# Kernel optimization log

Hardware: AMD Instinct MI355X
Metric: run time of the kernel (lower is better)

## Reference

```python
import jax
import jax.numpy as jnp
import numpy as np

B, S, D, H, HID, E, TOPK = 1, 2048, 1024, 16, 4096, 8, 2
HEAD_DIM = D // H


def _layer_norm(x, g, b, eps=1e-5):
    mu = jnp.mean(x, axis=-1, keepdims=True)
    var = jnp.var(x, axis=-1, keepdims=True)
    return (x - mu) * jax.lax.rsqrt(var + eps) * g + b


def setup_inputs() -> dict:
    key = jax.random.key(0)
    ks = jax.random.split(key, 12)
    s = 0.02
    return {
        "x": jax.random.normal(ks[0], (B, S, D), jnp.float32),
        "ln1_g": jnp.ones((D,), jnp.float32),
        "ln1_b": jnp.zeros((D,), jnp.float32),
        "wq": jax.random.normal(ks[1], (D, D), jnp.float32) * s,
        "wk": jax.random.normal(ks[2], (D, D), jnp.float32) * s,
        "wv": jax.random.normal(ks[3], (D, D), jnp.float32) * s,
        "wo": jax.random.normal(ks[4], (D, D), jnp.float32) * s,
        "ln2_g": jnp.ones((D,), jnp.float32),
        "ln2_b": jnp.zeros((D,), jnp.float32),
        "w_gate": jax.random.normal(ks[5], (D, E), jnp.float32) * s,
        "w_eg": jax.random.normal(ks[6], (E, D, HID), jnp.float32) * s,
        "w_eu": jax.random.normal(ks[7], (E, D, HID), jnp.float32) * s,
        "w_ed": jax.random.normal(ks[8], (E, HID, D), jnp.float32) * s,
    }


def _attention(h, wq, wk, wv, wo):
    b, s, d = h.shape
    q = (h @ wq).reshape(b, s, H, HEAD_DIM).transpose(0, 2, 1, 3)
    k = (h @ wk).reshape(b, s, H, HEAD_DIM).transpose(0, 2, 1, 3)
    v = (h @ wv).reshape(b, s, H, HEAD_DIM).transpose(0, 2, 1, 3)
    scores = jnp.einsum("bhqd,bhkd->bhqk", q, k) / jnp.sqrt(jnp.asarray(HEAD_DIM, h.dtype))
    causal = jnp.tril(jnp.ones((s, s), bool))  # [s,s]
    scores = jnp.where(causal, scores, jnp.asarray(-1e30, h.dtype))
    attn = jax.nn.softmax(scores, axis=-1)
    out = jnp.einsum("bhqk,bhkd->bhqd", attn, v).transpose(0, 2, 1, 3).reshape(b, s, d)
    return out @ wo


def _moe(h, w_gate, w_eg, w_eu, w_ed):
    b, s, d = h.shape
    flat = h.reshape(-1, d)  # [T,D]
    logits = flat @ w_gate  # [T,E]
    scores = jax.nn.sigmoid(logits)
    top_val, top_idx = jax.lax.top_k(scores, TOPK)
    top_val = top_val / (jnp.sum(top_val, axis=-1, keepdims=True) + 1e-9)
    # per-token per-expert combine weight (0 for unrouted experts)
    combine = jnp.sum(jax.nn.one_hot(top_idx, E, dtype=flat.dtype) * top_val[..., None], axis=1)  # [T,E]
    g = jax.nn.silu(jnp.einsum("td,edh->eth", flat, w_eg))
    u = jnp.einsum("td,edh->eth", flat, w_eu)
    eo = jnp.einsum("eth,ehd->etd", g * u, w_ed)  # [E,T,D]
    out = jnp.einsum("etd,te->td", eo, combine)
    return out.reshape(b, s, d)


def reference(x, ln1_g, ln1_b, wq, wk, wv, wo, ln2_g, ln2_b, w_gate, w_eg, w_eu, w_ed):
    x = x + _attention(_layer_norm(x, ln1_g, ln1_b), wq, wk, wv, wo)
    x = x + _moe(_layer_norm(x, ln2_g, ln2_b), w_gate, w_eg, w_eu, w_ed)
    return x
```

## Files before the change

### kernel.cpp

```cpp
#include <hip/hip_runtime.h>
#include <hip/hip_bf16.h>
#include <stdint.h>

#define DI __device__ __forceinline__

typedef short bf16x8_t __attribute__((ext_vector_type(8)));
typedef float f32x4_t __attribute__((ext_vector_type(4)));

DI unsigned short f2bf(float f) {
  __hip_bfloat16 h = __float2bfloat16(f);
  unsigned short u;
  __builtin_memcpy(&u, &h, 2);
  return u;
}

DI uint32_t pk2(float a, float b) {
  return (uint32_t)f2bf(a) | ((uint32_t)f2bf(b) << 16);
}

DI f32x4_t mfma16(bf16x8_t a, bf16x8_t b, f32x4_t c) {
  return __builtin_amdgcn_mfma_f32_16x16x32_bf16(a, b, c, 0, 0, 0);
}

DI void gload16(const void* g, void* l) {
  __builtin_amdgcn_global_load_lds(
      (const __attribute__((address_space(1))) uint32_t*)g,
      (__attribute__((address_space(3))) uint32_t*)l, 16, 0, 0);
}

DI bf16x8_t frag(const unsigned short* base, int row, int hi) {
  return *(const bf16x8_t*)&base[row * 32 + ((hi ^ ((row >> 1) & 3)) * 8)];
}
DI int chunk_swz(int tid) { return ((tid & 3) ^ ((tid >> 3) & 3)) * 8; }

__global__ __launch_bounds__(256) void transpose_cvt(const float* __restrict__ in,
                                                     unsigned short* __restrict__ out,
                                                     int R, int C) {
  __shared__ float tile[64][65];
  const int tid = threadIdx.x;
  const int tx = tid & 15, ty = tid >> 4;
  const size_t zoff = (size_t)blockIdx.z * R * C;
  const int r0 = blockIdx.y * 64, c0 = blockIdx.x * 64;
#pragma unroll
  for (int i = 0; i < 4; ++i) {
    const int r = ty + i * 16;
    const float4 v = *(const float4*)(in + zoff + (size_t)(r0 + r) * C + c0 + tx * 4);
    tile[r][tx * 4 + 0] = v.x; tile[r][tx * 4 + 1] = v.y;
    tile[r][tx * 4 + 2] = v.z; tile[r][tx * 4 + 3] = v.w;
  }
  __syncthreads();
#pragma unroll
  for (int i = 0; i < 4; ++i) {
    const int r = ty + i * 16;
    ushort4 o;
    o.x = f2bf(tile[tx * 4 + 0][r]); o.y = f2bf(tile[tx * 4 + 1][r]);
    o.z = f2bf(tile[tx * 4 + 2][r]); o.w = f2bf(tile[tx * 4 + 3][r]);
    *(ushort4*)(out + zoff + (size_t)(c0 + r) * R + r0 + tx * 4) = o;
  }
}

__global__ __launch_bounds__(256) void ln_kernel(const float* __restrict__ x, const float* __restrict__ g,
                                                 const float* __restrict__ b, unsigned short* __restrict__ out) {
  const int row = blockIdx.x, tid = threadIdx.x;
  const int wid = tid >> 6, lane = tid & 63;
  const float4 v = *(const float4*)(x + (size_t)row * 1024 + tid * 4);
  float s = v.x + v.y + v.z + v.w;
  float s2 = v.x * v.x + v.y * v.y + v.z * v.z + v.w * v.w;
#pragma unroll
  for (int o = 1; o < 64; o <<= 1) { s += __shfl_xor(s, o); s2 += __shfl_xor(s2, o); }
  __shared__ float red[8];
  if (lane == 0) { red[wid] = s; red[4 + wid] = s2; }
  __syncthreads();
  const float ts = red[0] + red[1] + red[2] + red[3];
  const float ts2 = red[4] + red[5] + red[6] + red[7];
  const float mu = ts * 0.0009765625f;
  const float var = ts2 * 0.0009765625f - mu * mu;
  const float rs = rsqrtf(var + 1e-5f);
  const float4 gg = *(const float4*)(g + tid * 4);
  const float4 bb = *(const float4*)(b + tid * 4);
  ushort4 o4;
  o4.x = f2bf((v.x - mu) * rs * gg.x + bb.x);
  o4.y = f2bf((v.y - mu) * rs * gg.y + bb.y);
  o4.z = f2bf((v.z - mu) * rs * gg.z + bb.z);
  o4.w = f2bf((v.w - mu) * rs * gg.w + bb.w);
  *(ushort4*)(out + (size_t)row * 1024 + tid * 4) = o4;
}

template<int BN>
DI void gemm_loop(const unsigned short* aR0, const unsigned short* aR1,
                  const unsigned short* bR0, const unsigned short* bR1,
                  const int K, unsigned short* lds, const int tid,
                  f32x4_t (&acc)[4][BN / 32]) {
  constexpr int NF = BN / 32;
  unsigned short* ldsA = lds;
  unsigned short* ldsB = lds + 4096;
  const int wid = tid >> 6, lane = tid & 63, ln = lane & 15, hi = lane >> 4;
  const int wr = wid >> 1, wc = wid & 1;
  char* dstA0 = (char*)ldsA + wid * 1024;
  char* dstA1 = (char*)ldsA + 4096 + wid * 1024;
  char* dstB0 = (char*)ldsB + wid * 1024;
  char* dstB1 = (char*)ldsB + 4096 + wid * 1024;
  for (int k0 = 0; k0 < K; k0 += 32) {
    gload16(aR0 + k0, dstA0);
    gload16(aR1 + k0, dstA1);
    gload16(bR0 + k0, dstB0);
    if constexpr (BN == 128) gload16(bR1 + k0, dstB1);
    __syncthreads();
    bf16x8_t af[4];
#pragma unroll
    for (int mf = 0; mf < 4; ++mf)
      af[mf] = frag(ldsA, wr * 64 + mf * 16 + ln, hi);
#pragma unroll
    for (int nf = 0; nf < NF; ++nf) {
      bf16x8_t bfr = frag(ldsB, wc * (BN / 2) + nf * 16 + ln, hi);
#pragma unroll
      for (int mf = 0; mf < 4; ++mf)
        acc[mf][nf] = mfma16(af[mf], bfr, acc[mf][nf]);
    }
    __syncthreads();
  }
}

__global__ __launch_bounds__(256) void qkv_kernel(const unsigned short* __restrict__ h1,
                                                  const unsigned short* __restrict__ wqT,
                                                  const unsigned short* __restrict__ wkT,
                                                  const unsigned short* __restrict__ wvT,
                                                  unsigned short* __restrict__ qb,
                                                  unsigned short* __restrict__ kbf,
                                                  unsigned short* __restrict__ vt) {
  __shared__ unsigned short lds[128 * 32 + 128 * 32];
  const int tid = threadIdx.x;
  const int z = blockIdx.z;
  const unsigned short* BT = (z == 0) ? wqT : (z == 1) ? wkT : wvT;
  const int m0 = blockIdx.y * 128, n0 = blockIdx.x * 128;
  f32x4_t acc[4][4] = {};
  const int cs = chunk_swz(tid);
  const unsigned short* aR0 = h1 + (size_t)(m0 + (tid >> 2)) * 1024 + cs;
  const unsigned short* aR1 = aR0 + 64 * 1024;
  const unsigned short* bR0 = BT + (size_t)(n0 + (tid >> 2)) * 1024 + cs;
  const unsigned short* bR1 = bR0 + 64 * 1024;
  gemm_loop<128>(aR0, aR1, bR0, bR1, 1024, lds, tid, acc);
  const int lane = tid & 63, ln = lane & 15, hi = lane >> 4, wid = tid >> 6;
  const int wr = wid >> 1, wc = wid & 1;
  if (z < 2) {
    unsigned short* o = z ? kbf : qb;
#pragma unroll
    for (int mf = 0; mf < 4; ++mf)
#pragma unroll
      for (int nf = 0; nf < 4; ++nf)
#pragma unroll
        for (int r = 0; r < 4; ++r) {
          const int m = m0 + wr * 64 + mf * 16 + hi * 4 + r;
          const int n = n0 + wc * 64 + nf * 16 + ln;
          o[(size_t)m * 1024 + n] = f2bf(acc[mf][nf][r]);
        }
  } else {
#pragma unroll
    for (int mf = 0; mf < 4; ++mf)
#pragma unroll
      for (int nf = 0; nf < 4; ++nf) {
        const int n = n0 + wc * 64 + nf * 16 + ln;
        const int mb = m0 + wr * 64 + mf * 16 + hi * 4;
        ushort4 o;
        o.x = f2bf(acc[mf][nf][0]); o.y = f2bf(acc[mf][nf][1]);
        o.z = f2bf(acc[mf][nf][2]); o.w = f2bf(acc[mf][nf][3]);
        *(ushort4*)(vt + (size_t)n * 2048 + mb) = o;
      }
  }
}

__global__ __launch_bounds__(256) void wo_kernel(const unsigned short* __restrict__ ao,
                                                 const unsigned short* __restrict__ woT,
                                                 const float* __restrict__ x,
                                                 float* __restrict__ out) {
  __shared__ unsigned short lds[128 * 32 + 64 * 32];
  const int tid = threadIdx.x;
  const int m0 = blockIdx.y * 128, n0 = blockIdx.x * 64;
  f32x4_t acc[4][2] = {};
  const int cs = chunk_swz(tid);
  const unsigned short* aR0 = ao + (size_t)(m0 + (tid >> 2)) * 1024 + cs;
  const unsigned short* aR1 = aR0 + 64 * 1024;
  const unsigned short* bR0 = woT + (size_t)(n0 + (tid >> 2)) * 1024 + cs;
  gemm_loop<64>(aR0, aR1, bR0, nullptr, 1024, lds, tid, acc);
  const int lane = tid & 63, ln = lane & 15, hi = lane >> 4, wid = tid >> 6;
  const int wr = wid >> 1, wc = wid & 1;
#pragma unroll
  for (int mf = 0; mf < 4; ++mf)
#pragma unroll
    for (int nf = 0; nf < 2; ++nf)
#pragma unroll
      for (int r = 0; r < 4; ++r) {
        const int m = m0 + wr * 64 + mf * 16 + hi * 4 + r;
        const int n = n0 + wc * 32 + nf * 16 + ln;
        out[(size_t)m * 1024 + n] = acc[mf][nf][r] + x[(size_t)m * 1024 + n];
      }
}

__global__ __launch_bounds__(256) void attn_kernel(const unsigned short* __restrict__ qb,
                                                   const unsigned short* __restrict__ kbuf,
                                                   const unsigned short* __restrict__ vt,
                                                   unsigned short* __restrict__ ao) {
  __shared__ unsigned short kTl[4096];
  __shared__ unsigned short vTl[4096];
  __shared__ unsigned short pl[4][1024];
  const int tid = threadIdx.x;
  const int wid = tid >> 6, lane = tid & 63;
  const int ln = lane & 15, hi = lane >> 4;
  const int h = blockIdx.y;
  const int q0 = blockIdx.x * 64;
  const int q0w = q0 + wid * 16;

  const unsigned short* qrow = qb + (size_t)(q0w + ln) * 1024 + h * 64 + hi * 8;
  const bf16x8_t aq0 = *(const bf16x8_t*)(qrow);
  const bf16x8_t aq1 = *(const bf16x8_t*)(qrow + 32);

  const int str_r = tid >> 3, str_c = tid & 7;
  const int swc = (str_c ^ (str_r & 7)) * 8;
  const unsigned short* ksrc0 = kbuf + (size_t)str_r * 1024 + h * 64 + swc;
  const unsigned short* ksrc1 = kbuf + (size_t)(str_r + 32) * 1024 + h * 64 + swc;
  const unsigned short* vsrc0 = vt + (size_t)(h * 64 + str_r) * 2048 + swc;
  const unsigned short* vsrc1 = vt + (size_t)(h * 64 + str_r + 32) * 2048 + swc;
  char* kd0 = (char*)kTl + wid * 1024;
  char* kd1 = (char*)kTl + 4096 + wid * 1024;
  char* vd0 = (char*)vTl + wid * 1024;
  char* vd1 = (char*)vTl + 4096 + wid * 1024;

  float m_r[4], l_r[4];
  f32x4_t o_acc[4] = {};
#pragma unroll
  for (int r = 0; r < 4; ++r) { m_r[r] = -1e30f; l_r[r] = 0.f; }

  const int nkv = blockIdx.x + 1;
  for (int it = 0; it < nkv; ++it) {
    const int kv0 = it * 64;
    gload16(ksrc0 + (size_t)kv0 * 1024, kd0);
    gload16(ksrc1 + (size_t)kv0 * 1024, kd1);
    gload16(vsrc0 + kv0, vd0);
    gload16(vsrc1 + kv0, vd1);
    __syncthreads();

    float sc[4][4];
#pragma unroll
    for (int cf = 0; cf < 4; ++cf) {
      const int row = cf * 16 + ln;
      const int swz = row & 7;
      const bf16x8_t b0 = *(const bf16x8_t*)((char*)kTl + row * 128 + ((hi ^ swz) * 16));
      const bf16x8_t b1 = *(const bf16x8_t*)((char*)kTl + row * 128 + (((4 + hi) ^ swz) * 16));
      f32x4_t zacc = {};
      zacc = mfma16(aq0, b0, zacc);
      zacc = mfma16(aq1, b1, zacc);
#pragma unroll
      for (int r = 0; r < 4; ++r) sc[cf][r] = zacc[r] * 0.125f;
    }
    if (kv0 + 63 > q0w) {
#pragma unroll
      for (int cf = 0; cf < 4; ++cf)
#pragma unroll
        for (int r = 0; r < 4; ++r) {
          const int qg = q0w + hi * 4 + r;
          const int kg = kv0 + cf * 16 + ln;
          if (kg > qg) sc[cf][r] = -1e30f;
        }
    }
#pragma unroll
    for (int r = 0; r < 4; ++r) {
      float tm = fmaxf(fmaxf(sc[0][r], sc[1][r]), fmaxf(sc[2][r], sc[3][r]));
      tm = fmaxf(tm, __shfl_xor(tm, 1));
      tm = fmaxf(tm, __shfl_xor(tm, 2));
      tm = fmaxf(tm, __shfl_xor(tm, 4));
      tm = fmaxf(tm, __shfl_xor(tm, 8));
      const float mn = fmaxf(m_r[r], tm);
      const float alpha = __expf(m_r[r] - mn);
      float rsum = 0.f;
#pragma unroll
      for (int cf = 0; cf < 4; ++cf) {
        const float p = __expf(sc[cf][r] - mn);
        sc[cf][r] = p; rsum += p;
      }
      rsum += __shfl_xor(rsum, 1); rsum += __shfl_xor(rsum, 2);
      rsum += __shfl_xor(rsum, 4); rsum += __shfl_xor(rsum, 8);
      l_r[r] = l_r[r] * alpha + rsum;
      m_r[r] = mn;
#pragma unroll
      for (int df = 0; df < 4; ++df) o_acc[df][r] *= alpha;
    }
    unsigned short* pw = &pl[wid][0];
#pragma unroll
    for (int cf = 0; cf < 4; ++cf)
#pragma unroll
      for (int r = 0; r < 4; ++r) {
        const int qq = hi * 4 + r;
        const int kv = cf * 16 + ln;
        const int bo = (qq * 128 + kv * 2) ^ ((qq & 7) << 4);
        *(unsigned short*)((char*)pw + bo) = f2bf(sc[cf][r]);
      }
    __syncthreads();
    const bf16x8_t pa0 = *(const bf16x8_t*)((char*)pw + ((ln * 128 + hi * 16) ^ ((ln & 7) << 4)));
    const bf16x8_t pa1 = *(const bf16x8_t*)((char*)pw + ((ln * 128 + 64 + hi * 16) ^ ((ln & 7) << 4)));
#pragma unroll
    for (int df = 0; df < 4; ++df) {
      const int d = df * 16 + ln;
      const int swz = d & 7;
      const bf16x8_t bv0 = *(const bf16x8_t*)((char*)vTl + d * 128 + ((hi ^ swz) * 16));
      const bf16x8_t bv1 = *(const bf16x8_t*)((char*)vTl + d * 128 + (((4 + hi) ^ swz) * 16));
      o_acc[df] = mfma16(pa0, bv0, o_acc[df]);
      o_acc[df] = mfma16(pa1, bv1, o_acc[df]);
    }
    __syncthreads();
  }
#pragma unroll
  for (int df = 0; df < 4; ++df) {
    const int n = h * 64 + df * 16 + ln;
#pragma unroll
    for (int r = 0; r < 4; ++r) {
      const int m = q0w + hi * 4 + r;
      ao[(size_t)m * 1024 + n] = f2bf(o_acc[df][r] / l_r[r]);
    }
  }
}

__global__ __launch_bounds__(256) void gate_kernel(const float* __restrict__ x2, const float* __restrict__ g,
                                                   const float* __restrict__ b, const float* __restrict__ wg,
                                                   int2* __restrict__ te, float2* __restrict__ tw,
                                                   int* __restrict__ cnt) {
  const int tid = threadIdx.x, wid = tid >> 6, lane = tid & 63;
  const int t = blockIdx.x * 4 + wid;
  const float* row = x2 + (size_t)t * 1024;
  float vv[16];
#pragma unroll
  for (int i = 0; i < 4; ++i) *(float4*)&vv[i * 4] = *(const float4*)(row + lane * 16 + i * 4);
  float s = 0.f, s2 = 0.f;
#pragma unroll
  for (int j = 0; j < 16; ++j) { s += vv[j]; s2 += vv[j] * vv[j]; }
#pragma unroll
  for (int o = 1; o < 64; o <<= 1) { s += __shfl_xor(s, o); s2 += __shfl_xor(s2, o); }
  const float mu = s * 0.0009765625f;
  const float var = s2 * 0.0009765625f - mu * mu;
  const float rs = rsqrtf(var + 1e-5f);
  float acc[8] = {0.f, 0.f, 0.f, 0.f, 0.f, 0.f, 0.f, 0.f};
#pragma unroll
  for (int j = 0; j < 16; ++j) {
    const int d = lane * 16 + j;
    const float xv = (vv[j] - mu) * rs * g[d] + b[d];
    const float4 w0 = *(const float4*)(wg + d * 8);
    const float4 w1 = *(const float4*)(wg + d * 8 + 4);
    acc[0] += xv * w0.x; acc[1] += xv * w0.y; acc[2] += xv * w0.z; acc[3] += xv * w0.w;
    acc[4] += xv * w1.x; acc[5] += xv * w1.y; acc[6] += xv * w1.z; acc[7] += xv * w1.w;
  }
#pragma unroll
  for (int o = 1; o < 64; o <<= 1) {
#pragma unroll
    for (int e = 0; e < 8; ++e) acc[e] += __shfl_xor(acc[e], o);
  }
  if (lane == 0) {
    float sg[8];
#pragma unroll
    for (int e = 0; e < 8; ++e) sg[e] = 1.f / (1.f + __expf(-acc[e]));
    int e0 = 0;
#pragma unroll
    for (int e = 1; e < 8; ++e) if (sg[e] > sg[e0]) e0 = e;
    int e1 = (e0 == 0) ? 1 : 0;
#pragma unroll
    for (int e = 0; e < 8; ++e) if (e != e0 && sg[e] > sg[e1]) e1 = e;
    const float v0 = sg[e0], v1 = sg[e1];
    const float inv = 1.f / (v0 + v1 + 1e-9f);
    te[t] = make_int2(e0, e1);
    tw[t] = make_float2(v0 * inv, v1 * inv);
    atomicAdd(&cnt[e0], 1);
    atomicAdd(&cnt[e1], 1);
  }
}

__global__ void zero_counters(int* p) { if (threadIdx.x < 8) p[threadIdx.x] = 0; }

__global__ __launch_bounds__(256) void g2_kernel(const int* __restrict__ cnt, int* __restrict__ slot_off,
                                                 int* __restrict__ tile_expert, int* __restrict__ tile_rowbase,
                                                 int* __restrict__ cursor, int* __restrict__ assign_token,
                                                 float* __restrict__ assign_w) {
  const int tid = threadIdx.x;
  for (int i = tid; i < 8192; i += 256) { assign_token[i] = -1; assign_w[i] = 0.f; }
  if (tid == 0) {
    int base = 0, tiles = 0;
    for (int e = 0; e < 8; ++e) {
      const int c = cnt[e];
      slot_off[e] = base;
      cursor[e] = 0;
      const int nt = (c + 255) >> 8;
      for (int i = 0; i < nt; ++i) {
        tile_expert[tiles] = e;
        tile_rowbase[tiles] = base + i * 256;
        ++tiles;
      }
      base += nt * 256;
    }
    for (; tiles < 40; ++tiles) tile_expert[tiles] = -1;
  }
}

__global__ __launch_bounds__(256) void g3_kernel(const int2* __restrict__ te, const float2* __restrict__ tw,
                                                 const int* __restrict__ slot_off, int* __restrict__ cursor,
                                                 int* __restrict__ assign_token, float* __restrict__ assign_w) {
  const int t = blockIdx.x * 256 + threadIdx.x;
  const int2 e = te[t];
  const float2 w = tw[t];
  const int s0 = slot_off[e.x] + atomicAdd(&cursor[e.x], 1);
  assign_token[s0] = t; assign_w[s0] = w.x;
  const int s1 = slot_off[e.y] + atomicAdd(&cursor[e.y], 1);
  assign_token[s1] = t; assign_w[s1] = w.y;
}

DI void stageA4(const unsigned short* a0, const unsigned short* a1,
                const unsigned short* a2, const unsigned short* a3,
                int koff, char* Ab, int wid) {
  gload16(a0 + koff, Ab + wid * 1024);
  gload16(a1 + koff, Ab + 4096 + wid * 1024);
  gload16(a2 + koff, Ab + 8192 + wid * 1024);
  gload16(a3 + koff, Ab + 12288 + wid * 1024);
}

DI void ug_write_b(char* Bn, const int* boff, const float4& q0, const float4& q1,
                   const float4& q2, const float4& q3) {
  const float* q0p = (const float*)&q0; const float* q1p = (const float*)&q1;
  const float* q2p = (const float*)&q2; const float* q3p = (const float*)&q3;
#pragma unroll
  for (int i = 0; i < 4; ++i) {
    uint2 w;
    w.x = pk2(q0p[i], q1p[i]);
    w.y = pk2(q2p[i], q3p[i]);
    *(uint2*)(Bn + boff[i]) = w;
  }
}

DI void ug_mfma256(const unsigned short* A, const char* Bb, int wr, int wc, int ln, int hi,
                   f32x4_t (&accg)[8][2], f32x4_t (&accu)[8][2]) {
  bf16x8_t af[8];
#pragma unroll
  for (int mf = 0; mf < 8; ++mf)
    af[mf] = frag(A, wr * 128 + mf * 16 + ln, hi);
#pragma unroll
  for (int nf = 0; nf < 2; ++nf) {
    const int nrow = wc * 32 + nf * 16 + ln;
    int bo = nrow * 64 + hi * 16;
    bo ^= ((nrow >> 2) & 7) << 4;
    const bf16x8_t bg = *(const bf16x8_t*)(Bb + bo);
    const bf16x8_t bu = *(const bf16x8_t*)(Bb + 4096 + bo);
#pragma unroll
    for (int mf = 0; mf < 8; ++mf) {
      accg[mf][nf] = mfma16(af[mf], bg, accg[mf][nf]);
      accu[mf][nf] = mfma16(af[mf], bu, accu[mf][nf]);
    }
  }
}

__global__ __launch_bounds__(256, 2) void upgate_kernel(const unsigned short* __restrict__ h2,
                                                        const float* __restrict__ w_eg, const float* __restrict__ w_eu,
                                                        const int* __restrict__ tile_expert,
                                                        const int* __restrict__ tile_rowbase,
                                                        const int* __restrict__ assign_token,
                                                        unsigned short* __restrict__ act) {
  const int by = blockIdx.y;
  const int e = tile_expert[by];
  if (e < 0) return;
  const int n0 = blockIdx.x * 64;
  const int rowbase = tile_rowbase[by];
  const int tid = threadIdx.x;
  __shared__ unsigned short lds[2 * 8192 + 2 * 4096];
  char* A0 = (char*)lds;
  char* A1 = (char*)lds + 16384;
  char* B0 = (char*)lds + 32768;
  char* B1 = (char*)lds + 40960;
  const int wid = tid >> 6, lane = tid & 63, ln = lane & 15, hi = lane >> 4;
  const int wr = wid >> 1, wc = wid & 1;
  const int r0s = rowbase + (tid >> 2);
  int tk0 = assign_token[r0s];        tk0 = tk0 < 0 ? 0 : tk0;
  int tk1 = assign_token[r0s + 64];   tk1 = tk1 < 0 ? 0 : tk1;
  int tk2 = assign_token[r0s + 128];  tk2 = tk2 < 0 ? 0 : tk2;
  int tk3 = assign_token[r0s + 192];  tk3 = tk3 < 0 ? 0 : tk3;
  const int cs = chunk_swz(tid);
  const unsigned short* aR0 = h2 + (size_t)tk0 * 1024 + cs;
  const unsigned short* aR1 = h2 + (size_t)tk1 * 1024 + cs;
  const unsigned short* aR2 = h2 + (size_t)tk2 * 1024 + cs;
  const unsigned short* aR3 = h2 + (size_t)tk3 * 1024 + cs;
  const int mat = tid >> 7;
  const int blk = tid & 127;
  const int kb = (blk >> 4) * 4;
  const int nb = (blk & 15) * 4;
  const float* bsrc = (mat ? w_eu : w_eg) + (size_t)e * 1024 * 4096 + (size_t)kb * 4096 + n0 + nb;
  int boff[4];
#pragma unroll
  for (int i = 0; i < 4; ++i) {
    const int n = nb + i;
    int bo = mat * 4096 + n * 64 + kb * 2;
    bo ^= ((n >> 2) & 7) << 4;
    boff[i] = bo;
  }
  f32x4_t accg[8][2] = {};
  f32x4_t accu[8][2] = {};
  float4 qA0, qA1, qA2, qA3, qB0, qB1, qB2, qB3;
  qB0 = *(const float4*)(bsrc);
  qB1 = *(const float4*)(bsrc + 4096);
  qB2 = *(const float4*)(bsrc + 8192);
  qB3 = *(const float4*)(bsrc + 12288);
  stageA4(aR0, aR1, aR2, aR3, 0, A0, wid);
  __builtin_amdgcn_sched_barrier(0);
  ug_write_b(B0, boff, qB0, qB1, qB2, qB3);
  {
    const float* bs = bsrc + (size_t)32 * 4096;
    qA0 = *(const float4*)(bs);
    qA1 = *(const float4*)(bs + 4096);
    qA2 = *(const float4*)(bs + 8192);
    qA3 = *(const float4*)(bs + 12288);
  }
  stageA4(aR0, aR1, aR2, aR3, 32, A1, wid);
  asm volatile("s_waitcnt vmcnt(8)" ::: "memory");
  __builtin_amdgcn_sched_barrier(0);
  asm volatile("s_waitcnt lgkmcnt(0)" ::: "memory");
  __builtin_amdgcn_sched_barrier(0);
  __builtin_amdgcn_s_barrier();
  for (int p = 0; p < 15; ++p) {
    {
      const int t = 2 * p;
      const float* bs = bsrc + (size_t)(t + 2) * 32 * 4096;
      qB0 = *(const float4*)(bs);
      qB1 = *(const float4*)(bs + 4096);
      qB2 = *(const float4*)(bs + 8192);
      qB3 = *(const float4*)(bs + 12288);
      stageA4(aR0, aR1, aR2, aR3, (t + 1) * 32, A1, wid);
      __builtin_amdgcn_sched_barrier(0);
      ug_write_b(B1, boff, qA0, qA1, qA2, qA3);
      ug_mfma256((const unsigned short*)A0, B0, wr, wc, ln, hi, accg, accu);
      asm volatile("s_waitcnt vmcnt(4)" ::: "memory");
      __builtin_amdgcn_sched_barrier(0);
      asm volatile("s_waitcnt lgkmcnt(0)" ::: "memory");
      __builtin_amdgcn_sched_barrier(0);
      __builtin_amdgcn_s_barrier();
    }
    {
      const int t = 2 * p + 1;
      const float* bs = bsrc + (size_t)(t + 2) * 32 * 4096;
      qA0 = *(const float4*)(bs);
      qA1 = *(const float4*)(bs + 4096);
      qA2 = *(const float4*)(bs + 8192);
      qA3 = *(const float4*)(bs + 12288);
      stageA4(aR0, aR1, aR2, aR3, (t + 1) * 32, A0, wid);
      __builtin_amdgcn_sched_barrier(0);
      ug_write_b(B0, boff, qB0, qB1, qB2, qB3);
      ug_mfma256((const unsigned short*)A1, B1, wr, wc, ln, hi, accg, accu);
      asm volatile("s_waitcnt vmcnt(4)" ::: "memory");
      __builtin_amdgcn_sched_barrier(0);
      asm volatile("s_waitcnt lgkmcnt(0)" ::: "memory");
      __builtin_amdgcn_sched_barrier(0);
      __builtin_amdgcn_s_barrier();
    }
  }
  stageA4(aR0, aR1, aR2, aR3, 31 * 32, A1, wid);
  __builtin_amdgcn_sched_barrier(0);
  ug_write_b(B1, boff, qA0, qA1, qA2, qA3);
  ug_mfma256((const unsigned short*)A0, B0, wr, wc, ln, hi, accg, accu);
  asm volatile("s_waitcnt vmcnt(0)" ::: "memory");
  __builtin_amdgcn_sched_barrier(0);
  asm volatile("s_waitcnt lgkmcnt(0)" ::: "memory");
  __builtin_amdgcn_sched_barrier(0);
  __builtin_amdgcn_s_barrier();
  ug_mfma256((const unsigned short*)A1, B1, wr, wc, ln, hi, accg, accu);
#pragma unroll
  for (int mf = 0; mf < 8; ++mf)
#pragma unroll
    for (int nf = 0; nf < 2; ++nf)
#pragma unroll
      for (int r = 0; r < 4; ++r) {
        const int m = wr * 128 + mf * 16 + hi * 4 + r;
        const int n = n0 + wc * 32 + nf * 16 + ln;
        const float gv = accg[mf][nf][r], uv = accu[mf][nf][r];
        const float val = gv / (1.f + __expf(-gv)) * uv;
        act[(size_t)(rowbase + m) * 4096 + n] = f2bf(val);
      }
}

DI void dn_write_b(char* Bn, const int* boff, const float4& q0, const float4& q1) {
  const float* q0p = (const float*)&q0; const float* q1p = (const float*)&q1;
#pragma unroll
  for (int i = 0; i < 4; ++i)
    *(uint32_t*)(Bn + boff[i]) = pk2(q0p[i], q1p[i]);
}

DI void dn_mfma256(const unsigned short* A, const char* Bb, int wr, int wc, int ln, int hi,
                   f32x4_t (&acc)[8][2]) {
  bf16x8_t af[8];
#pragma unroll
  for (int mf = 0; mf < 8; ++mf)
    af[mf] = frag(A, wr * 128 + mf * 16 + ln, hi);
#pragma unroll
  for (int nf = 0; nf < 2; ++nf) {
    const int nrow = wc * 32 + nf * 16 + ln;
    int bo = nrow * 64 + hi * 16;
    bo ^= ((nrow >> 2) & 7) << 4;
    const bf16x8_t bb = *(const bf16x8_t*)(Bb + bo);
#pragma unroll
    for (int mf = 0; mf < 8; ++mf)
      acc[mf][nf] = mfma16(af[mf], bb, acc[mf][nf]);
  }
}

__global__ __launch_bounds__(256, 2) void down_kernel(const unsigned short* __restrict__ act,
                                                      const float* __restrict__ w_ed,
                                                      const int* __restrict__ tile_expert,
                                                      const int* __restrict__ tile_rowbase,
                                                      const int* __restrict__ assign_token,
                                                      const float* __restrict__ assign_w,
                                                      float* __restrict__ out) {
  const int by = blockIdx.y;
  const int e = tile_expert[by];
  if (e < 0) return;
  const int n0 = blockIdx.x * 64;
  const int rowbase = tile_rowbase[by];
  const int tid = threadIdx.x;
  __shared__ unsigned short lds[2 * 8192 + 2 * 2048];
  char* A0 = (char*)lds;
  char* A1 = (char*)lds + 16384;
  char* B0 = (char*)lds + 32768;
  char* B1 = (char*)lds + 36864;
  const int wid = tid >> 6, lane = tid & 63, ln = lane & 15, hi = lane >> 4;
  const int wr = wid >> 1, wc = wid & 1;
  const int cs = chunk_swz(tid);
  const unsigned short* aR0 = act + (size_t)(rowbase + (tid >> 2)) * 4096 + cs;
  const unsigned short* aR1 = aR0 + (size_t)64 * 4096;
  const unsigned short* aR2 = aR0 + (size_t)128 * 4096;
  const unsigned short* aR3 = aR0 + (size_t)192 * 4096;
  const int nb = (tid & 15) * 4;
  const int kb2 = (tid >> 4) * 2;
  const float* bsrc = w_ed + (size_t)e * 4096 * 1024 + (size_t)kb2 * 1024 + n0 + nb;
  int boff[4];
#pragma unroll
  for (int i = 0; i < 4; ++i) {
    const int n = nb + i;
    int bo = n * 64 + kb2 * 2;
    bo ^= ((n >> 2) & 7) << 4;
    boff[i] = bo;
  }
  f32x4_t acc[8][2] = {};
  float4 qA0, qA1, qB0, qB1;
  qB0 = *(const float4*)(bsrc);
  qB1 = *(const float4*)(bsrc + 1024);
  stageA4(aR0, aR1, aR2, aR3, 0, A0, wid);
  __builtin_amdgcn_sched_barrier(0);
  dn_write_b(B0, boff, qB0, qB1);
  {
    const float* bs = bsrc + (size_t)32 * 1024;
    qA0 = *(const float4*)(bs);
    qA1 = *(const float4*)(bs + 1024);
  }
  stageA4(aR0, aR1, aR2, aR3, 32, A1, wid);
  asm volatile("s_waitcnt vmcnt(6)" ::: "memory");
  __builtin_amdgcn_sched_barrier(0);
  asm volatile("s_waitcnt lgkmcnt(0)" ::: "memory");
  __builtin_amdgcn_sched_barrier(0);
  __builtin_amdgcn_s_barrier();
  for (int p = 0; p < 63; ++p) {
    {
      const int t = 2 * p;
      const float* bs = bsrc + (size_t)(t + 2) * 32 * 1024;
      qB0 = *(const float4*)(bs);
      qB1 = *(const float4*)(bs + 1024);
      stageA4(aR0, aR1, aR2, aR3, (t + 1) * 32, A1, wid);
      __builtin_amdgcn_sched_barrier(0);
      dn_write_b(B1, boff, qA0, qA1);
      dn_mfma256((const unsigned short*)A0, B0, wr, wc, ln, hi, acc);
      asm volatile("s_waitcnt vmcnt(2)" ::: "memory");
      __builtin_amdgcn_sched_barrier(0);
      asm volatile("s_waitcnt lgkmcnt(0)" ::: "memory");
      __builtin_amdgcn_sched_barrier(0);
      __builtin_amdgcn_s_barrier();
    }
    {
      const int t = 2 * p + 1;
      const float* bs = bsrc + (size_t)(t + 2) * 32 * 1024;
      qA0 = *(const float4*)(bs);
      qA1 = *(const float4*)(bs + 1024);
      stageA4(aR0, aR1, aR2, aR3, (t + 1) * 32, A0, wid);
      __builtin_amdgcn_sched_barrier(0);
      dn_write_b(B0, boff, qB0, qB1);
      dn_mfma256((const unsigned short*)A1, B1, wr, wc, ln, hi, acc);
      asm volatile("s_waitcnt vmcnt(2)" ::: "memory");
      __builtin_amdgcn_sched_barrier(0);
      asm volatile("s_waitcnt lgkmcnt(0)" ::: "memory");
      __builtin_amdgcn_sched_barrier(0);
      __builtin_amdgcn_s_barrier();
    }
  }
  stageA4(aR0, aR1, aR2, aR3, 127 * 32, A1, wid);
  __builtin_amdgcn_sched_barrier(0);
  dn_write_b(B1, boff, qA0, qA1);
  dn_mfma256((const unsigned short*)A0, B0, wr, wc, ln, hi, acc);
  asm volatile("s_waitcnt vmcnt(0)" ::: "memory");
  __builtin_amdgcn_sched_barrier(0);
  asm volatile("s_waitcnt lgkmcnt(0)" ::: "memory");
  __builtin_amdgcn_sched_barrier(0);
  __builtin_amdgcn_s_barrier();
  dn_mfma256((const unsigned short*)A1, B1, wr, wc, ln, hi, acc);
#pragma unroll
  for (int mf = 0; mf < 8; ++mf)
#pragma unroll
    for (int r = 0; r < 4; ++r) {
      const int m = wr * 128 + mf * 16 + hi * 4 + r;
      const int slot = rowbase + m;
      const int tk = assign_token[slot];
      if (tk >= 0) {
        const float w = assign_w[slot];
#pragma unroll
        for (int nf = 0; nf < 2; ++nf) {
          const int n = n0 + wc * 32 + nf * 16 + ln;
          atomicAdd(out + (size_t)tk * 1024 + n, acc[mf][nf][r] * w);
        }
      }
    }
}

extern "C" void kernel_launch(void* const* d_in, const int* in_sizes, int n_in,
                              void* d_out, int out_size, void* d_ws, size_t ws_size,
                              hipStream_t stream) {
  (void)in_sizes; (void)n_in; (void)out_size;
  const float* x    = (const float*)d_in[0];
  const float* ln1g = (const float*)d_in[1];
  const float* ln1b = (const float*)d_in[2];
  const float* wq   = (const float*)d_in[3];
  const float* wk   = (const float*)d_in[4];
  const float* wv   = (const float*)d_in[5];
  const float* wo   = (const float*)d_in[6];
  const float* ln2g = (const float*)d_in[7];
  const float* ln2b = (const float*)d_in[8];
  const float* wg   = (const float*)d_in[9];
  const float* weg  = (const float*)d_in[10];
  const float* weu  = (const float*)d_in[11];
  const float* wed  = (const float*)d_in[12];
  float* out = (float*)d_out;
  char* ws = (char*)d_ws;

  const size_t MB = (size_t)1 << 20;
  if (ws_size < 86 * MB) return;
  unsigned short* wqT = (unsigned short*)(ws + 0 * MB);
  unsigned short* wkT = (unsigned short*)(ws + 2 * MB);
  unsigned short* wvT = (unsigned short*)(ws + 4 * MB);
  unsigned short* woT = (unsigned short*)(ws + 6 * MB);
  unsigned short* h1  = (unsigned short*)(ws + 8 * MB);
  unsigned short* qb  = (unsigned short*)(ws + 12 * MB);
  unsigned short* kbf = (unsigned short*)(ws + 16 * MB);
  unsigned short* vt  = (unsigned short*)(ws + 20 * MB);
  unsigned short* ao  = (unsigned short*)(ws + 24 * MB);
  unsigned short* h2  = (unsigned short*)(ws + 28 * MB);
  unsigned short* act = (unsigned short*)(ws + 32 * MB);
  int2*   te = (int2*)(ws + 84 * MB);
  float2* tw = (float2*)(ws + 84 * MB + 16384);
  int*  meta = (int*)(ws + 84 * MB + 32768);
  int* cnt = meta;
  int* cursor = meta + 8;
  int* slot_off = meta + 16;
  int* tile_expert = meta + 24;
  int* tile_rowbase = meta + 64;
  int*   assign_token = (int*)(ws + 84 * MB + 36864);
  float* assign_w     = (float*)(ws + 84 * MB + 36864 + 32768);

  zero_counters<<<1, 64, 0, stream>>>(cnt);
  transpose_cvt<<<dim3(16, 16, 1), 256, 0, stream>>>(wq, wqT, 1024, 1024);
  transpose_cvt<<<dim3(16, 16, 1), 256, 0, stream>>>(wk, wkT, 1024, 1024);
  transpose_cvt<<<dim3(16, 16, 1), 256, 0, stream>>>(wv, wvT, 1024, 1024);
  transpose_cvt<<<dim3(16, 16, 1), 256, 0, stream>>>(wo, woT, 1024, 1024);
  ln_kernel<<<2048, 256, 0, stream>>>(x, ln1g, ln1b, h1);
  qkv_kernel<<<dim3(8, 16, 3), 256, 0, stream>>>(h1, wqT, wkT, wvT, qb, kbf, vt);
  attn_kernel<<<dim3(32, 16), 256, 0, stream>>>(qb, kbf, vt, ao);
  wo_kernel<<<dim3(16, 16), 256, 0, stream>>>(ao, woT, x, out);
  ln_kernel<<<2048, 256, 0, stream>>>(out, ln2g, ln2b, h2);
  gate_kernel<<<512, 256, 0, stream>>>(out, ln2g, ln2b, wg, te, tw, cnt);
  g2_kernel<<<1, 256, 0, stream>>>(cnt, slot_off, tile_expert, tile_rowbase, cursor, assign_token, assign_w);
  g3_kernel<<<8, 256, 0, stream>>>(te, tw, slot_off, cursor, assign_token, assign_w);
  upgate_kernel<<<dim3(64, 24), 256, 0, stream>>>(h2, weg, weu, tile_expert, tile_rowbase, assign_token, act);
  down_kernel<<<dim3(16, 24), 256, 0, stream>>>(act, wed, tile_expert, tile_rowbase, assign_token, assign_w, out);
}
```

Baseline: 524.7 us.

## Split down-projection into 128-row tiles with split-K over four K chunks

The down-projection kernel now uses 128-row tiles (each 256-row expert tile is split in two) and a split-K grid dimension of 4, so each block handles 1024 of the 4096 hidden channels. The grid grows from 16x24 to 16x48x4 blocks and per-block LDS and accumulators shrink, which is meant to fix under-occupancy of the GPU in the down GEMM. Partial sums are combined through the existing atomicAdd into the output, which multiplies atomic traffic by four and reloads the weight tile twice as often. The A-tile prefetch is also reordered to issue before the B global loads in both kernels, and the extra initial A stage with its vmcnt wait is dropped.

```diff
diff --git a/kernel.cpp b/kernel.cpp
--- a/kernel.cpp
+++ b/kernel.cpp
@@ -416,6 +416,11 @@
   gload16(a1 + koff, Ab + 4096 + wid * 1024);
   gload16(a2 + koff, Ab + 8192 + wid * 1024);
   gload16(a3 + koff, Ab + 12288 + wid * 1024);
+}
+DI void stageA2(const unsigned short* a0, const unsigned short* a1,
+                int koff, char* Ab, int wid) {
+  gload16(a0 + koff, Ab + wid * 1024);
+  gload16(a1 + koff, Ab + 4096 + wid * 1024);
 }
 
 DI void ug_write_b(char* Bn, const int* boff, const float4& q0, const float4& q1,
@@ -497,11 +502,11 @@
   f32x4_t accg[8][2] = {};
   f32x4_t accu[8][2] = {};
   float4 qA0, qA1, qA2, qA3, qB0, qB1, qB2, qB3;
+  stageA4(aR0, aR1, aR2, aR3, 0, A0, wid);
   qB0 = *(const float4*)(bsrc);
   qB1 = *(const float4*)(bsrc + 4096);
   qB2 = *(const float4*)(bsrc + 8192);
   qB3 = *(const float4*)(bsrc + 12288);
-  stageA4(aR0, aR1, aR2, aR3, 0, A0, wid);
   __builtin_amdgcn_sched_barrier(0);
   ug_write_b(B0, boff, qB0, qB1, qB2, qB3);
   {
@@ -511,21 +516,18 @@
     qA2 = *(const float4*)(bs + 8192);
     qA3 = *(const float4*)(bs + 12288);
   }
-  stageA4(aR0, aR1, aR2, aR3, 32, A1, wid);
-  asm volatile("s_waitcnt vmcnt(8)" ::: "memory");
-  __builtin_amdgcn_sched_barrier(0);
   asm volatile("s_waitcnt lgkmcnt(0)" ::: "memory");
   __builtin_amdgcn_sched_barrier(0);
   __builtin_amdgcn_s_barrier();
   for (int p = 0; p < 15; ++p) {
     {
       const int t = 2 * p;
+      stageA4(aR0, aR1, aR2, aR3, (t + 1) * 32, A1, wid);
       const float* bs = bsrc + (size_t)(t + 2) * 32 * 4096;
       qB0 = *(const float4*)(bs);
       qB1 = *(const float4*)(bs + 4096);
       qB2 = *(const float4*)(bs + 8192);
       qB3 = *(const float4*)(bs + 12288);
-      stageA4(aR0, aR1, aR2, aR3, (t + 1) * 32, A1, wid);
       __builtin_amdgcn_sched_barrier(0);
       ug_write_b(B1, boff, qA0, qA1, qA2, qA3);
       ug_mfma256((const unsigned short*)A0, B0, wr, wc, ln, hi, accg, accu);
@@ -537,12 +539,12 @@
     }
     {
       const int t = 2 * p + 1;
+      stageA4(aR0, aR1, aR2, aR3, (t + 1) * 32, A0, wid);
       const float* bs = bsrc + (size_t)(t + 2) * 32 * 4096;
       qA0 = *(const float4*)(bs);
       qA1 = *(const float4*)(bs + 4096);
       qA2 = *(const float4*)(bs + 8192);
       qA3 = *(const float4*)(bs + 12288);
-      stageA4(aR0, aR1, aR2, aR3, (t + 1) * 32, A0, wid);
       __builtin_amdgcn_sched_barrier(0);
       ug_write_b(B0, boff, qB0, qB1, qB2, qB3);
       ug_mfma256((const unsigned short*)A1, B1, wr, wc, ln, hi, accg, accu);
@@ -584,12 +586,12 @@
     *(uint32_t*)(Bn + boff[i]) = pk2(q0p[i], q1p[i]);
 }
 
-DI void dn_mfma256(const unsigned short* A, const char* Bb, int wr, int wc, int ln, int hi,
-                   f32x4_t (&acc)[8][2]) {
-  bf16x8_t af[8];
-#pragma unroll
-  for (int mf = 0; mf < 8; ++mf)
-    af[mf] = frag(A, wr * 128 + mf * 16 + ln, hi);
+DI void dn_mfma(const unsigned short* A, const char* Bb, int wr, int wc, int ln, int hi,
+                f32x4_t (&acc)[4][2]) {
+  bf16x8_t af[4];
+#pragma unroll
+  for (int mf = 0; mf < 4; ++mf)
+    af[mf] = frag(A, wr * 64 + mf * 16 + ln, hi);
 #pragma unroll
   for (int nf = 0; nf < 2; ++nf) {
     const int nrow = wc * 32 + nf * 16 + ln;
@@ -597,39 +599,38 @@
     bo ^= ((nrow >> 2) & 7) << 4;
     const bf16x8_t bb = *(const bf16x8_t*)(Bb + bo);
 #pragma unroll
-    for (int mf = 0; mf < 8; ++mf)
+    for (int mf = 0; mf < 4; ++mf)
       acc[mf][nf] = mfma16(af[mf], bb, acc[mf][nf]);
   }
 }
 
-__global__ __launch_bounds__(256, 2) void down_kernel(const unsigned short* __restrict__ act,
-                                                      const float* __restrict__ w_ed,
-                                                      const int* __restrict__ tile_expert,
-                                                      const int* __restrict__ tile_rowbase,
-                                                      const int* __restrict__ assign_token,
-                                                      const float* __restrict__ assign_w,
-                                                      float* __restrict__ out) {
-  const int by = blockIdx.y;
-  const int e = tile_expert[by];
+__global__ __launch_bounds__(256) void down_kernel(const unsigned short* __restrict__ act,
+                                                   const float* __restrict__ w_ed,
+                                                   const int* __restrict__ tile_expert,
+                                                   const int* __restrict__ tile_rowbase,
+                                                   const int* __restrict__ assign_token,
+                                                   const float* __restrict__ assign_w,
+                                                   float* __restrict__ out) {
+  const int tix = blockIdx.y;
+  const int e = tile_expert[tix >> 1];
   if (e < 0) return;
+  const int rowbase = tile_rowbase[tix >> 1] + (tix & 1) * 128;
   const int n0 = blockIdx.x * 64;
-  const int rowbase = tile_rowbase[by];
+  const int kz = blockIdx.z * 1024;
   const int tid = threadIdx.x;
-  __shared__ unsigned short lds[2 * 8192 + 2 * 2048];
+  __shared__ unsigned short lds[2 * 4096 + 2 * 2048];
   char* A0 = (char*)lds;
-  char* A1 = (char*)lds + 16384;
-  char* B0 = (char*)lds + 32768;
-  char* B1 = (char*)lds + 36864;
+  char* A1 = (char*)lds + 8192;
+  char* B0 = (char*)lds + 16384;
+  char* B1 = (char*)lds + 20480;
   const int wid = tid >> 6, lane = tid & 63, ln = lane & 15, hi = lane >> 4;
   const int wr = wid >> 1, wc = wid & 1;
   const int cs = chunk_swz(tid);
-  const unsigned short* aR0 = act + (size_t)(rowbase + (tid >> 2)) * 4096 + cs;
+  const unsigned short* aR0 = act + (size_t)(rowbase + (tid >> 2)) * 4096 + kz + cs;
   const unsigned short* aR1 = aR0 + (size_t)64 * 4096;
-  const unsigned short* aR2 = aR0 + (size_t)128 * 4096;
-  const unsigned short* aR3 = aR0 + (size_t)192 * 4096;
   const int nb = (tid & 15) * 4;
   const int kb2 = (tid >> 4) * 2;
-  const float* bsrc = w_ed + (size_t)e * 4096 * 1024 + (size_t)kb2 * 1024 + n0 + nb;
+  const float* bsrc = w_ed + (size_t)e * 4096 * 1024 + (size_t)(kz + kb2) * 1024 + n0 + nb;
   int boff[4];
 #pragma unroll
   for (int i = 0; i < 4; ++i) {
@@ -638,11 +639,11 @@
     bo ^= ((n >> 2) & 7) << 4;
     boff[i] = bo;
   }
-  f32x4_t acc[8][2] = {};
+  f32x4_t acc[4][2] = {};
   float4 qA0, qA1, qB0, qB1;
+  stageA2(aR0, aR1, 0, A0, wid);
   qB0 = *(const float4*)(bsrc);
   qB1 = *(const float4*)(bsrc + 1024);
-  stageA4(aR0, aR1, aR2, aR3, 0, A0, wid);
   __builtin_amdgcn_sched_barrier(0);
   dn_write_b(B0, boff, qB0, qB1);
   {
@@ -650,22 +651,19 @@
     qA0 = *(const float4*)(bs);
     qA1 = *(const float4*)(bs + 1024);
   }
-  stageA4(aR0, aR1, aR2, aR3, 32, A1, wid);
-  asm volatile("s_waitcnt vmcnt(6)" ::: "memory");
-  __builtin_amdgcn_sched_barrier(0);
   asm volatile("s_waitcnt lgkmcnt(0)" ::: "memory");
   __builtin_amdgcn_sched_barrier(0);
   __builtin_amdgcn_s_barrier();
-  for (int p = 0; p < 63; ++p) {
+  for (int p = 0; p < 15; ++p) {
     {
       const int t = 2 * p;
+      stageA2(aR0, aR1, (t + 1) * 32, A1, wid);
       const float* bs = bsrc + (size_t)(t + 2) * 32 * 1024;
       qB0 = *(const float4*)(bs);
       qB1 = *(const float4*)(bs + 1024);
-      stageA4(aR0, aR1, aR2, aR3, (t + 1) * 32, A1, wid);
       __builtin_amdgcn_sched_barrier(0);
       dn_write_b(B1, boff, qA0, qA1);
-      dn_mfma256((const unsigned short*)A0, B0, wr, wc, ln, hi, acc);
+      dn_mfma((const unsigned short*)A0, B0, wr, wc, ln, hi, acc);
       asm volatile("s_waitcnt vmcnt(2)" ::: "memory");
       __builtin_amdgcn_sched_barrier(0);
       asm volatile("s_waitcnt lgkmcnt(0)" ::: "memory");
@@ -674,13 +672,13 @@
     }
     {
       const int t = 2 * p + 1;
+      stageA2(aR0, aR1, (t + 1) * 32, A0, wid);
       const float* bs = bsrc + (size_t)(t + 2) * 32 * 1024;
       qA0 = *(const float4*)(bs);
       qA1 = *(const float4*)(bs + 1024);
-      stageA4(aR0, aR1, aR2, aR3, (t + 1) * 32, A0, wid);
       __builtin_amdgcn_sched_barrier(0);
       dn_write_b(B0, boff, qB0, qB1);
-      dn_mfma256((const unsigned short*)A1, B1, wr, wc, ln, hi, acc);
+      dn_mfma((const unsigned short*)A1, B1, wr, wc, ln, hi, acc);
       asm volatile("s_waitcnt vmcnt(2)" ::: "memory");
       __builtin_amdgcn_sched_barrier(0);
       asm volatile("s_waitcnt lgkmcnt(0)" ::: "memory");
@@ -688,21 +686,21 @@
       __builtin_amdgcn_s_barrier();
     }
   }
-  stageA4(aR0, aR1, aR2, aR3, 127 * 32, A1, wid);
+  stageA2(aR0, aR1, 31 * 32, A1, wid);
   __builtin_amdgcn_sched_barrier(0);
   dn_write_b(B1, boff, qA0, qA1);
-  dn_mfma256((const unsigned short*)A0, B0, wr, wc, ln, hi, acc);
+  dn_mfma((const unsigned short*)A0, B0, wr, wc, ln, hi, acc);
   asm volatile("s_waitcnt vmcnt(0)" ::: "memory");
   __builtin_amdgcn_sched_barrier(0);
   asm volatile("s_waitcnt lgkmcnt(0)" ::: "memory");
   __builtin_amdgcn_sched_barrier(0);
   __builtin_amdgcn_s_barrier();
-  dn_mfma256((const unsigned short*)A1, B1, wr, wc, ln, hi, acc);
-#pragma unroll
-  for (int mf = 0; mf < 8; ++mf)
+  dn_mfma((const unsigned short*)A1, B1, wr, wc, ln, hi, acc);
+#pragma unroll
+  for (int mf = 0; mf < 4; ++mf)
 #pragma unroll
     for (int r = 0; r < 4; ++r) {
-      const int m = wr * 128 + mf * 16 + hi * 4 + r;
+      const int m = wr * 64 + mf * 16 + hi * 4 + r;
       const int slot = rowbase + m;
       const int tk = assign_token[slot];
       if (tk >= 0) {
@@ -774,5 +772,5 @@
   g2_kernel<<<1, 256, 0, stream>>>(cnt, slot_off, tile_expert, tile_rowbase, cursor, assign_token, assign_w);
   g3_kernel<<<8, 256, 0, stream>>>(te, tw, slot_off, cursor, assign_token, assign_w);
   upgate_kernel<<<dim3(64, 24), 256, 0, stream>>>(h2, weg, weu, tile_expert, tile_rowbase, assign_token, act);
-  down_kernel<<<dim3(16, 24), 256, 0, stream>>>(act, wed, tile_expert, tile_rowbase, assign_token, assign_w, out);
-}
+  down_kernel<<<dim3(16, 48, 4), 256, 0, stream>>>(act, wed, tile_expert, tile_rowbase, assign_token, assign_w, out);
+}
```

After: 495.7 us. 1.06x faster.

## Split-K the MoE down projection, merge transposes, raise MFMA priority

Applied to the files above, without the earlier changes.

The MoE down-projection kernel gains a 4-way split over the hidden (K) dimension through blockIdx.z. Each block now loops over 1024 of the K values instead of 4096, which quadruples the grid and should fill the GPU better. The four weight transpose launches are merged into one launch over a z grid dimension. s_setprio is raised around MFMA sections in the GEMM, attention, upgate and down kernels, and the A-tile prefetch is moved ahead of the B loads, dropping a prologue stage and its vmcnt wait. Split-K depends on the down epilogue accumulating into the output atomically, and adds more partial-sum traffic to that output.

```diff
diff --git a/kernel.cpp b/kernel.cpp
--- a/kernel.cpp
+++ b/kernel.cpp
@@ -33,18 +33,21 @@
 }
 DI int chunk_swz(int tid) { return ((tid & 3) ^ ((tid >> 3) & 3)) * 8; }
 
-__global__ __launch_bounds__(256) void transpose_cvt(const float* __restrict__ in,
-                                                     unsigned short* __restrict__ out,
-                                                     int R, int C) {
+__global__ __launch_bounds__(256) void transpose_cvt4(const float* __restrict__ s0, const float* __restrict__ s1,
+                                                      const float* __restrict__ s2, const float* __restrict__ s3,
+                                                      unsigned short* __restrict__ d0, unsigned short* __restrict__ d1,
+                                                      unsigned short* __restrict__ d2, unsigned short* __restrict__ d3) {
   __shared__ float tile[64][65];
+  const int z = blockIdx.z;
+  const float* in = (z == 0) ? s0 : (z == 1) ? s1 : (z == 2) ? s2 : s3;
+  unsigned short* out = (z == 0) ? d0 : (z == 1) ? d1 : (z == 2) ? d2 : d3;
   const int tid = threadIdx.x;
   const int tx = tid & 15, ty = tid >> 4;
-  const size_t zoff = (size_t)blockIdx.z * R * C;
   const int r0 = blockIdx.y * 64, c0 = blockIdx.x * 64;
 #pragma unroll
   for (int i = 0; i < 4; ++i) {
     const int r = ty + i * 16;
-    const float4 v = *(const float4*)(in + zoff + (size_t)(r0 + r) * C + c0 + tx * 4);
+    const float4 v = *(const float4*)(in + (size_t)(r0 + r) * 1024 + c0 + tx * 4);
     tile[r][tx * 4 + 0] = v.x; tile[r][tx * 4 + 1] = v.y;
     tile[r][tx * 4 + 2] = v.z; tile[r][tx * 4 + 3] = v.w;
   }
@@ -55,7 +58,7 @@
     ushort4 o;
     o.x = f2bf(tile[tx * 4 + 0][r]); o.y = f2bf(tile[tx * 4 + 1][r]);
     o.z = f2bf(tile[tx * 4 + 2][r]); o.w = f2bf(tile[tx * 4 + 3][r]);
-    *(ushort4*)(out + zoff + (size_t)(c0 + r) * R + r0 + tx * 4) = o;
+    *(ushort4*)(out + (size_t)(c0 + r) * 1024 + r0 + tx * 4) = o;
   }
 }
 
@@ -110,6 +113,7 @@
 #pragma unroll
     for (int mf = 0; mf < 4; ++mf)
       af[mf] = frag(ldsA, wr * 64 + mf * 16 + ln, hi);
+    __builtin_amdgcn_s_setprio(1);
 #pragma unroll
     for (int nf = 0; nf < NF; ++nf) {
       bf16x8_t bfr = frag(ldsB, wc * (BN / 2) + nf * 16 + ln, hi);
@@ -117,6 +121,7 @@
       for (int mf = 0; mf < 4; ++mf)
         acc[mf][nf] = mfma16(af[mf], bfr, acc[mf][nf]);
     }
+    __builtin_amdgcn_s_setprio(0);
     __syncthreads();
   }
 }
@@ -240,6 +245,7 @@
     __syncthreads();
 
     float sc[4][4];
+    __builtin_amdgcn_s_setprio(1);
 #pragma unroll
     for (int cf = 0; cf < 4; ++cf) {
       const int row = cf * 16 + ln;
@@ -252,6 +258,7 @@
 #pragma unroll
       for (int r = 0; r < 4; ++r) sc[cf][r] = zacc[r] * 0.125f;
     }
+    __builtin_amdgcn_s_setprio(0);
     if (kv0 + 63 > q0w) {
 #pragma unroll
       for (int cf = 0; cf < 4; ++cf)
@@ -297,6 +304,7 @@
     __syncthreads();
     const bf16x8_t pa0 = *(const bf16x8_t*)((char*)pw + ((ln * 128 + hi * 16) ^ ((ln & 7) << 4)));
     const bf16x8_t pa1 = *(const bf16x8_t*)((char*)pw + ((ln * 128 + 64 + hi * 16) ^ ((ln & 7) << 4)));
+    __builtin_amdgcn_s_setprio(1);
 #pragma unroll
     for (int df = 0; df < 4; ++df) {
       const int d = df * 16 + ln;
@@ -306,6 +314,7 @@
       o_acc[df] = mfma16(pa0, bv0, o_acc[df]);
       o_acc[df] = mfma16(pa1, bv1, o_acc[df]);
     }
+    __builtin_amdgcn_s_setprio(0);
     __syncthreads();
   }
 #pragma unroll
@@ -437,6 +446,7 @@
 #pragma unroll
   for (int mf = 0; mf < 8; ++mf)
     af[mf] = frag(A, wr * 128 + mf * 16 + ln, hi);
+  __builtin_amdgcn_s_setprio(1);
 #pragma unroll
   for (int nf = 0; nf < 2; ++nf) {
     const int nrow = wc * 32 + nf * 16 + ln;
@@ -450,6 +460,7 @@
       accu[mf][nf] = mfma16(af[mf], bu, accu[mf][nf]);
     }
   }
+  __builtin_amdgcn_s_setprio(0);
 }
 
 __global__ __launch_bounds__(256, 2) void upgate_kernel(const unsigned short* __restrict__ h2,
@@ -497,11 +508,11 @@
   f32x4_t accg[8][2] = {};
   f32x4_t accu[8][2] = {};
   float4 qA0, qA1, qA2, qA3, qB0, qB1, qB2, qB3;
+  stageA4(aR0, aR1, aR2, aR3, 0, A0, wid);
   qB0 = *(const float4*)(bsrc);
   qB1 = *(const float4*)(bsrc + 4096);
   qB2 = *(const float4*)(bsrc + 8192);
   qB3 = *(const float4*)(bsrc + 12288);
-  stageA4(aR0, aR1, aR2, aR3, 0, A0, wid);
   __builtin_amdgcn_sched_barrier(0);
   ug_write_b(B0, boff, qB0, qB1, qB2, qB3);
   {
@@ -511,21 +522,18 @@
     qA2 = *(const float4*)(bs + 8192);
     qA3 = *(const float4*)(bs + 12288);
   }
-  stageA4(aR0, aR1, aR2, aR3, 32, A1, wid);
-  asm volatile("s_waitcnt vmcnt(8)" ::: "memory");
-  __builtin_amdgcn_sched_barrier(0);
   asm volatile("s_waitcnt lgkmcnt(0)" ::: "memory");
   __builtin_amdgcn_sched_barrier(0);
   __builtin_amdgcn_s_barrier();
   for (int p = 0; p < 15; ++p) {
     {
       const int t = 2 * p;
+      stageA4(aR0, aR1, aR2, aR3, (t + 1) * 32, A1, wid);
       const float* bs = bsrc + (size_t)(t + 2) * 32 * 4096;
       qB0 = *(const float4*)(bs);
       qB1 = *(const float4*)(bs + 4096);
       qB2 = *(const float4*)(bs + 8192);
       qB3 = *(const float4*)(bs + 12288);
-      stageA4(aR0, aR1, aR2, aR3, (t + 1) * 32, A1, wid);
       __builtin_amdgcn_sched_barrier(0);
       ug_write_b(B1, boff, qA0, qA1, qA2, qA3);
       ug_mfma256((const unsigned short*)A0, B0, wr, wc, ln, hi, accg, accu);
@@ -537,12 +545,12 @@
     }
     {
       const int t = 2 * p + 1;
+      stageA4(aR0, aR1, aR2, aR3, (t + 1) * 32, A0, wid);
       const float* bs = bsrc + (size_t)(t + 2) * 32 * 4096;
       qA0 = *(const float4*)(bs);
       qA1 = *(const float4*)(bs + 4096);
       qA2 = *(const float4*)(bs + 8192);
       qA3 = *(const float4*)(bs + 12288);
-      stageA4(aR0, aR1, aR2, aR3, (t + 1) * 32, A0, wid);
       __builtin_amdgcn_sched_barrier(0);
       ug_write_b(B0, boff, qB0, qB1, qB2, qB3);
       ug_mfma256((const unsigned short*)A1, B1, wr, wc, ln, hi, accg, accu);
@@ -590,6 +598,7 @@
 #pragma unroll
   for (int mf = 0; mf < 8; ++mf)
     af[mf] = frag(A, wr * 128 + mf * 16 + ln, hi);
+  __builtin_amdgcn_s_setprio(1);
 #pragma unroll
   for (int nf = 0; nf < 2; ++nf) {
     const int nrow = wc * 32 + nf * 16 + ln;
@@ -600,6 +609,7 @@
     for (int mf = 0; mf < 8; ++mf)
       acc[mf][nf] = mfma16(af[mf], bb, acc[mf][nf]);
   }
+  __builtin_amdgcn_s_setprio(0);
 }
 
 __global__ __launch_bounds__(256, 2) void down_kernel(const unsigned short* __restrict__ act,
@@ -612,8 +622,9 @@
   const int by = blockIdx.y;
   const int e = tile_expert[by];
   if (e < 0) return;
+  const int rowbase = tile_rowbase[by];
   const int n0 = blockIdx.x * 64;
-  const int rowbase = tile_rowbase[by];
+  const int kz = blockIdx.z * 1024;
   const int tid = threadIdx.x;
   __shared__ unsigned short lds[2 * 8192 + 2 * 2048];
   char* A0 = (char*)lds;
@@ -623,13 +634,13 @@
   const int wid = tid >> 6, lane = tid & 63, ln = lane & 15, hi = lane >> 4;
   const int wr = wid >> 1, wc = wid & 1;
   const int cs = chunk_swz(tid);
-  const unsigned short* aR0 = act + (size_t)(rowbase + (tid >> 2)) * 4096 + cs;
+  const unsigned short* aR0 = act + (size_t)(rowbase + (tid >> 2)) * 4096 + kz + cs;
   const unsigned short* aR1 = aR0 + (size_t)64 * 4096;
   const unsigned short* aR2 = aR0 + (size_t)128 * 4096;
   const unsigned short* aR3 = aR0 + (size_t)192 * 4096;
   const int nb = (tid & 15) * 4;
   const int kb2 = (tid >> 4) * 2;
-  const float* bsrc = w_ed + (size_t)e * 4096 * 1024 + (size_t)kb2 * 1024 + n0 + nb;
+  const float* bsrc = w_ed + (size_t)e * 4096 * 1024 + (size_t)(kz + kb2) * 1024 + n0 + nb;
   int boff[4];
 #pragma unroll
   for (int i = 0; i < 4; ++i) {
@@ -640,9 +651,9 @@
   }
   f32x4_t acc[8][2] = {};
   float4 qA0, qA1, qB0, qB1;
+  stageA4(aR0, aR1, aR2, aR3, 0, A0, wid);
   qB0 = *(const float4*)(bsrc);
   qB1 = *(const float4*)(bsrc + 1024);
-  stageA4(aR0, aR1, aR2, aR3, 0, A0, wid);
   __builtin_amdgcn_sched_barrier(0);
   dn_write_b(B0, boff, qB0, qB1);
   {
@@ -650,19 +661,16 @@
     qA0 = *(const float4*)(bs);
     qA1 = *(const float4*)(bs + 1024);
   }
-  stageA4(aR0, aR1, aR2, aR3, 32, A1, wid);
-  asm volatile("s_waitcnt vmcnt(6)" ::: "memory");
-  __builtin_amdgcn_sched_barrier(0);
   asm volatile("s_waitcnt lgkmcnt(0)" ::: "memory");
   __builtin_amdgcn_sched_barrier(0);
   __builtin_amdgcn_s_barrier();
-  for (int p = 0; p < 63; ++p) {
+  for (int p = 0; p < 15; ++p) {
     {
       const int t = 2 * p;
+      stageA4(aR0, aR1, aR2, aR3, (t + 1) * 32, A1, wid);
       const float* bs = bsrc + (size_t)(t + 2) * 32 * 1024;
       qB0 = *(const float4*)(bs);
       qB1 = *(const float4*)(bs + 1024);
-      stageA4(aR0, aR1, aR2, aR3, (t + 1) * 32, A1, wid);
       __builtin_amdgcn_sched_barrier(0);
       dn_write_b(B1, boff, qA0, qA1);
       dn_mfma256((const unsigned short*)A0, B0, wr, wc, ln, hi, acc);
@@ -674,10 +682,10 @@
     }
     {
       const int t = 2 * p + 1;
+      stageA4(aR0, aR1, aR2, aR3, (t + 1) * 32, A0, wid);
       const float* bs = bsrc + (size_t)(t + 2) * 32 * 1024;
       qA0 = *(const float4*)(bs);
       qA1 = *(const float4*)(bs + 1024);
-      stageA4(aR0, aR1, aR2, aR3, (t + 1) * 32, A0, wid);
       __builtin_amdgcn_sched_barrier(0);
       dn_write_b(B0, boff, qB0, qB1);
       dn_mfma256((const unsigned short*)A1, B1, wr, wc, ln, hi, acc);
@@ -688,7 +696,7 @@
       __builtin_amdgcn_s_barrier();
     }
   }
-  stageA4(aR0, aR1, aR2, aR3, 127 * 32, A1, wid);
+  stageA4(aR0, aR1, aR2, aR3, 31 * 32, A1, wid);
   __builtin_amdgcn_sched_barrier(0);
   dn_write_b(B1, boff, qA0, qA1);
   dn_mfma256((const unsigned short*)A0, B0, wr, wc, ln, hi, acc);
@@ -761,10 +769,7 @@
   float* assign_w     = (float*)(ws + 84 * MB + 36864 + 32768);
 
   zero_counters<<<1, 64, 0, stream>>>(cnt);
-  transpose_cvt<<<dim3(16, 16, 1), 256, 0, stream>>>(wq, wqT, 1024, 1024);
-  transpose_cvt<<<dim3(16, 16, 1), 256, 0, stream>>>(wk, wkT, 1024, 1024);
-  transpose_cvt<<<dim3(16, 16, 1), 256, 0, stream>>>(wv, wvT, 1024, 1024);
-  transpose_cvt<<<dim3(16, 16, 1), 256, 0, stream>>>(wo, woT, 1024, 1024);
+  transpose_cvt4<<<dim3(16, 16, 4), 256, 0, stream>>>(wq, wk, wv, wo, wqT, wkT, wvT, woT);
   ln_kernel<<<2048, 256, 0, stream>>>(x, ln1g, ln1b, h1);
   qkv_kernel<<<dim3(8, 16, 3), 256, 0, stream>>>(h1, wqT, wkT, wvT, qb, kbf, vt);
   attn_kernel<<<dim3(32, 16), 256, 0, stream>>>(qb, kbf, vt, ao);
@@ -774,5 +779,5 @@
   g2_kernel<<<1, 256, 0, stream>>>(cnt, slot_off, tile_expert, tile_rowbase, cursor, assign_token, assign_w);
   g3_kernel<<<8, 256, 0, stream>>>(te, tw, slot_off, cursor, assign_token, assign_w);
   upgate_kernel<<<dim3(64, 24), 256, 0, stream>>>(h2, weg, weu, tile_expert, tile_rowbase, assign_token, act);
-  down_kernel<<<dim3(16, 24), 256, 0, stream>>>(act, wed, tile_expert, tile_rowbase, assign_token, assign_w, out);
-}
+  down_kernel<<<dim3(16, 24, 4), 256, 0, stream>>>(act, wed, tile_expert, tile_rowbase, assign_token, assign_w, out);
+}
```

Result: faster. 507.0 us (-3.4%).
